# Kernel optimization log

Hardware: AMD Instinct MI355X
Metric: run time of the kernel (lower is better)

## Reference

```python
import jax, jax.numpy as jnp
import numpy as np

EPS = 1e-6
SEARCH_RANGE = 4  # K = 2*R+1 = 9


def setup_inputs() -> dict:
    key = jax.random.key(0)
    k1, k2, k3, k4 = jax.random.split(key, 4)
    B, C, H, W = 4, 128, 128, 240
    E = 64
    F_L = jax.random.normal(k1, (B, C, H, W), dtype=jnp.float32)
    F_R = jax.random.normal(k2, (B, C, H, W), dtype=jnp.float32)
    d0 = jax.random.uniform(k3, (B, 1, H, W), dtype=jnp.float32) * 64.0  # pixel disparity
    phi_w = jax.random.normal(k4, (E, C), dtype=jnp.float32) / np.sqrt(C)  # 1x1 conv weight
    return {"F_L": F_L, "F_R": F_R, "d0": d0, "phi_w": phi_w}


def _embed(x, phi_w):
    # 1x1 conv + channel L2 normalize (cosine embedding)
    y = jnp.einsum('ec,bchw->behw', phi_w, x)
    norm = jnp.sqrt(jnp.sum(y * y, axis=1, keepdims=True)) + EPS
    return y / norm


def reference(F_L, F_R, d0, phi_w):
    R = SEARCH_RANGE
    FL = _embed(F_L, phi_w)  # (B,E,H,W)
    FR = _embed(F_R, phi_w)
    B, E, H, W = FL.shape
    deltas = jnp.arange(-R, R + 1, dtype=FL.dtype)  # (K,)
    xx = jnp.arange(W, dtype=FL.dtype)  # base x grid
    # x' = x - (d0 + delta); align_corners=True grid round-trips to pixel coords exactly,
    # y coordinate is identity, so warp is 1D bilinear along W with border clamp.
    xprime = xx[None, None, None, :] - d0[:, None, 0, :, :] - deltas[None, :, None, None]  # (B,K,H,W)
    x0 = jnp.floor(xprime)
    w = xprime - x0  # bilinear weight
    i0 = jnp.clip(x0.astype(jnp.int32), 0, W - 1)
    i1 = jnp.clip(x0.astype(jnp.int32) + 1, 0, W - 1)
    FR_e = FR[:, None]  # (B,1,E,H,W)
    g0 = jnp.take_along_axis(FR_e, i0[:, :, None, :, :], axis=4)  # (B,K,E,H,W)
    g1 = jnp.take_along_axis(FR_e, i1[:, :, None, :, :], axis=4)
    FR_s = g0 * (1.0 - w)[:, :, None] + g1 * w[:, :, None]
    cost_vol = jnp.einsum('behw,bkehw->bkhw', FL, FR_s)  # (B,K,H,W)
    return cost_vol
```

## Files before the change

### kernel.cpp

```cpp
#include <hip/hip_runtime.h>

#define NB 4
#define NC 128
#define NH 128
#define NW 240
#define NE 64
#define NK 9
#define PLANE (NH*NW)
#define CHW (NC*PLANE)

typedef __attribute__((ext_vector_type(8))) short short8;
typedef __attribute__((ext_vector_type(4))) float f32x4;

__device__ __forceinline__ unsigned short f2bf(float f){
  unsigned u = __float_as_uint(f);
  u += 0x7fffu + ((u>>16)&1u);
  return (unsigned short)(u>>16);
}
__device__ __forceinline__ float bfl(unsigned v){ return __uint_as_float(v<<16); }
__device__ __forceinline__ float bfh(unsigned v){ return __uint_as_float(v & 0xffff0000u); }

__global__ __launch_bounds__(256, 1)
void corr_kernel(const float* __restrict__ xL,
                 const float* __restrict__ xR,
                 const float* __restrict__ d0g,
                 const float* __restrict__ phig,
                 float* __restrict__ outg)
{
  __shared__ __attribute__((aligned(16))) unsigned short stag[NW*136];
  __shared__ __attribute__((aligned(16))) unsigned short phis[NE*136];
  __shared__ __attribute__((aligned(16))) unsigned short FLb[NW*64];
  __shared__ __attribute__((aligned(16))) unsigned short FRb[NW*64];

  const int tid  = threadIdx.x;
  const int lane = tid & 63;
  const int wv   = tid >> 6;
  const int b    = blockIdx.x >> 7;
  const int h    = blockIdx.x & 127;
  const size_t base = (size_t)b*CHW + (size_t)h*NW;

  float4 le0[8], le1[8], lo0[8], lo1[8];
  #pragma unroll
  for (int i = 0; i < 8; ++i) {
    int tau = tid + 256*i;
    if (tau < 1920) {
      int c2 = tau & 63, wo = tau >> 6;
      size_t off = base + (size_t)(2*c2)*PLANE + 8*wo;
      le0[i] = *(const float4*)(xL + off);
      le1[i] = *(const float4*)(xL + off + 4);
      lo0[i] = *(const float4*)(xL + off + PLANE);
      lo1[i] = *(const float4*)(xL + off + PLANE + 4);
    }
  }
  float4 ph[8];
  #pragma unroll
  for (int i = 0; i < 8; ++i) {
    int tau = tid + 256*i;
    int row = tau >> 5, ch = tau & 31;
    ph[i] = *(const float4*)(phig + row*128 + 4*ch);
  }

  #pragma unroll
  for (int i = 0; i < 8; ++i) {
    int tau = tid + 256*i;
    int row = tau >> 5, ch = tau & 31;
    unsigned w0 = (unsigned)f2bf(ph[i].x) | ((unsigned)f2bf(ph[i].y) << 16);
    unsigned w1 = (unsigned)f2bf(ph[i].z) | ((unsigned)f2bf(ph[i].w) << 16);
    uint2 pk; pk.x = w0; pk.y = w1;
    *(uint2*)&phis[row*136 + 4*ch] = pk;
  }
  #pragma unroll
  for (int i = 0; i < 8; ++i) {
    int tau = tid + 256*i;
    if (tau < 1920) {
      int c2 = tau & 63, wo = tau >> 6;
      float fe[8] = {le0[i].x, le0[i].y, le0[i].z, le0[i].w,
                     le1[i].x, le1[i].y, le1[i].z, le1[i].w};
      float fo[8] = {lo0[i].x, lo0[i].y, lo0[i].z, lo0[i].w,
                     lo1[i].x, lo1[i].y, lo1[i].z, lo1[i].w};
      #pragma unroll
      for (int j = 0; j < 8; ++j) {
        unsigned v = (unsigned)f2bf(fe[j]) | ((unsigned)f2bf(fo[j]) << 16);
        *(unsigned*)&stag[(8*wo + j)*136 + 2*c2] = v;
      }
    }
  }
  __syncthreads();

  float4 re0[8], re1[8], ro0[8], ro1[8];
  #pragma unroll
  for (int i = 0; i < 8; ++i) {
    int tau = tid + 256*i;
    if (tau < 1920) {
      int c2 = tau & 63, wo = tau >> 6;
      size_t off = base + (size_t)(2*c2)*PLANE + 8*wo;
      re0[i] = *(const float4*)(xR + off);
      re1[i] = *(const float4*)(xR + off + 4);
      ro0[i] = *(const float4*)(xR + off + PLANE);
      ro1[i] = *(const float4*)(xR + off + PLANE + 4);
    }
  }

  const int mrow = lane & 15;
  const int kg   = lane >> 4;
  const int nt0  = wv*4;

  auto gemm_norm = [&](unsigned short* dst) {
    f32x4 acc[4][4];
    #pragma unroll
    for (int i = 0; i < 4; ++i)
      #pragma unroll
      for (int mt = 0; mt < 4; ++mt)
        acc[i][mt] = (f32x4){0.f,0.f,0.f,0.f};

    #pragma unroll
    for (int ks = 0; ks < 4; ++ks) {
      short8 af[4];
      #pragma unroll
      for (int mt = 0; mt < 4; ++mt)
        af[mt] = *(const short8*)&phis[(16*mt + mrow)*136 + 32*ks + 8*kg];
      #pragma unroll
      for (int i = 0; i < 4; ++i) {
        int nt = nt0 + i;
        if (nt < 15) {
          short8 bfv = *(const short8*)&stag[(16*nt + mrow)*136 + 32*ks + 8*kg];
          #pragma unroll
          for (int mt = 0; mt < 4; ++mt)
            acc[i][mt] = __builtin_amdgcn_mfma_f32_16x16x32_bf16(af[mt], bfv, acc[i][mt], 0, 0, 0);
        }
      }
    }
    #pragma unroll
    for (int i = 0; i < 4; ++i) {
      int nt = nt0 + i;
      if (nt >= 15) continue;
      float ss = 0.f;
      #pragma unroll
      for (int mt = 0; mt < 4; ++mt)
        #pragma unroll
        for (int r = 0; r < 4; ++r)
          ss += acc[i][mt][r]*acc[i][mt][r];
      ss += __shfl_xor(ss, 16, 64);
      ss += __shfl_xor(ss, 32, 64);
      float inv = 1.f/(sqrtf(ss) + 1e-6f);
      int n = 16*nt + mrow;
      #pragma unroll
      for (int mt = 0; mt < 4; ++mt) {
        int e0 = 16*mt + 4*kg;
        ushort4 pk;
        pk.x = f2bf(acc[i][mt][0]*inv);
        pk.y = f2bf(acc[i][mt][1]*inv);
        pk.z = f2bf(acc[i][mt][2]*inv);
        pk.w = f2bf(acc[i][mt][3]*inv);
        int pos = n*64 + (((e0>>3) ^ (n&7))<<3) + (e0&7);
        *(ushort4*)&dst[pos] = pk;
      }
    }
  };

  gemm_norm(FLb);
  __syncthreads();

  #pragma unroll
  for (int i = 0; i < 8; ++i) {
    int tau = tid + 256*i;
    if (tau < 1920) {
      int c2 = tau & 63, wo = tau >> 6;
      float fe[8] = {re0[i].x, re0[i].y, re0[i].z, re0[i].w,
                     re1[i].x, re1[i].y, re1[i].z, re1[i].w};
      float fo[8] = {ro0[i].x, ro0[i].y, ro0[i].z, ro0[i].w,
                     ro1[i].x, ro1[i].y, ro1[i].z, ro1[i].w};
      #pragma unroll
      for (int j = 0; j < 8; ++j) {
        unsigned v = (unsigned)f2bf(fe[j]) | ((unsigned)f2bf(fo[j]) << 16);
        *(unsigned*)&stag[(8*wo + j)*136 + 2*c2] = v;
      }
    }
  }
  __syncthreads();

  gemm_norm(FRb);
  __syncthreads();

  if (tid < NW) {
    const int p = tid;
    float d0v = d0g[(b*NH + h)*NW + p];
    float xf  = (float)p - d0v;
    float x0  = floorf(xf);
    float wfr = xf - x0;
    int jb = (int)x0 - 4;

    float fl[64];
    #pragma unroll
    for (int c = 0; c < 8; ++c) {
      uint4 raw = *(const uint4*)&FLb[p*64 + ((c ^ (p&7))<<3)];
      fl[8*c+0]=bfl(raw.x); fl[8*c+1]=bfh(raw.x);
      fl[8*c+2]=bfl(raw.y); fl[8*c+3]=bfh(raw.y);
      fl[8*c+4]=bfl(raw.z); fl[8*c+5]=bfh(raw.z);
      fl[8*c+6]=bfl(raw.w); fl[8*c+7]=bfh(raw.w);
    }

    float D[10];
    #pragma unroll
    for (int t = 0; t < 10; ++t) {
      int j = jb + t;
      j = j < 0 ? 0 : (j > NW-1 ? NW-1 : j);
      float s = 0.f;
      #pragma unroll
      for (int c = 0; c < 8; ++c) {
        uint4 raw = *(const uint4*)&FRb[j*64 + ((c ^ (j&7))<<3)];
        s += fl[8*c+0]*bfl(raw.x) + fl[8*c+1]*bfh(raw.x)
           + fl[8*c+2]*bfl(raw.y) + fl[8*c+3]*bfh(raw.y)
           + fl[8*c+4]*bfl(raw.z) + fl[8*c+5]*bfh(raw.z)
           + fl[8*c+6]*bfl(raw.w) + fl[8*c+7]*bfh(raw.w);
      }
      D[t] = s;
    }

    size_t ob = (size_t)(b*NK)*PLANE + (size_t)h*NW + p;
    #pragma unroll
    for (int k = 0; k < NK; ++k) {
      int t0 = 8 - k;
      float cv = (1.f - wfr)*D[t0] + wfr*D[t0+1];
      outg[ob + (size_t)k*PLANE] = cv;
    }
  }
}

extern "C" void kernel_launch(void* const* d_in, const int* in_sizes, int n_in,
                              void* d_out, int out_size, void* d_ws, size_t ws_size,
                              hipStream_t stream) {
  const float* xL   = (const float*)d_in[0];
  const float* xR   = (const float*)d_in[1];
  const float* d0g  = (const float*)d_in[2];
  const float* phig = (const float*)d_in[3];
  float* outg = (float*)d_out;
  corr_kernel<<<dim3(NB*NH), dim3(256), 0, stream>>>(xL, xR, d0g, phig, outg);
}
```

Baseline: 174.4 us.

## Stage inputs channel-major in LDS and gather MFMA B fragments per element

```diff
diff --git a/kernel.cpp b/kernel.cpp
--- a/kernel.cpp
+++ b/kernel.cpp
@@ -8,6 +8,7 @@
 #define NK 9
 #define PLANE (NH*NW)
 #define CHW (NC*PLANE)
+#define XS 244
 
 typedef __attribute__((ext_vector_type(8))) short short8;
 typedef __attribute__((ext_vector_type(4))) float f32x4;
@@ -27,7 +28,7 @@
                  const float* __restrict__ phig,
                  float* __restrict__ outg)
 {
-  __shared__ __attribute__((aligned(16))) unsigned short stag[NW*136];
+  __shared__ __attribute__((aligned(16))) unsigned short xs[NC*XS];
   __shared__ __attribute__((aligned(16))) unsigned short phis[NE*136];
   __shared__ __attribute__((aligned(16))) unsigned short FLb[NW*64];
   __shared__ __attribute__((aligned(16))) unsigned short FRb[NW*64];
@@ -39,67 +40,31 @@
   const int h    = blockIdx.x & 127;
   const size_t base = (size_t)b*CHW + (size_t)h*NW;
 
-  float4 le0[8], le1[8], lo0[8], lo1[8];
+  float d0v = 0.f;
+  if (tid < NW) d0v = d0g[(b*NH + h)*NW + tid];
+
   #pragma unroll
   for (int i = 0; i < 8; ++i) {
-    int tau = tid + 256*i;
-    if (tau < 1920) {
-      int c2 = tau & 63, wo = tau >> 6;
-      size_t off = base + (size_t)(2*c2)*PLANE + 8*wo;
-      le0[i] = *(const float4*)(xL + off);
-      le1[i] = *(const float4*)(xL + off + 4);
-      lo0[i] = *(const float4*)(xL + off + PLANE);
-      lo1[i] = *(const float4*)(xL + off + PLANE + 4);
-    }
-  }
-  float4 ph[8];
+    int idx = i*256 + tid;
+    int e = idx >> 5, q = idx & 31;
+    float4 v = *(const float4*)(phig + e*128 + 4*q);
+    uint2 pk;
+    pk.x = (unsigned)f2bf(v.x) | ((unsigned)f2bf(v.y) << 16);
+    pk.y = (unsigned)f2bf(v.z) | ((unsigned)f2bf(v.w) << 16);
+    *(uint2*)&phis[e*136 + 4*q] = pk;
+  }
+
   #pragma unroll
-  for (int i = 0; i < 8; ++i) {
-    int tau = tid + 256*i;
-    int row = tau >> 5, ch = tau & 31;
-    ph[i] = *(const float4*)(phig + row*128 + 4*ch);
-  }
-
-  #pragma unroll
-  for (int i = 0; i < 8; ++i) {
-    int tau = tid + 256*i;
-    int row = tau >> 5, ch = tau & 31;
-    unsigned w0 = (unsigned)f2bf(ph[i].x) | ((unsigned)f2bf(ph[i].y) << 16);
-    unsigned w1 = (unsigned)f2bf(ph[i].z) | ((unsigned)f2bf(ph[i].w) << 16);
-    uint2 pk; pk.x = w0; pk.y = w1;
-    *(uint2*)&phis[row*136 + 4*ch] = pk;
-  }
-  #pragma unroll
-  for (int i = 0; i < 8; ++i) {
-    int tau = tid + 256*i;
-    if (tau < 1920) {
-      int c2 = tau & 63, wo = tau >> 6;
-      float fe[8] = {le0[i].x, le0[i].y, le0[i].z, le0[i].w,
-                     le1[i].x, le1[i].y, le1[i].z, le1[i].w};
-      float fo[8] = {lo0[i].x, lo0[i].y, lo0[i].z, lo0[i].w,
-                     lo1[i].x, lo1[i].y, lo1[i].z, lo1[i].w};
-      #pragma unroll
-      for (int j = 0; j < 8; ++j) {
-        unsigned v = (unsigned)f2bf(fe[j]) | ((unsigned)f2bf(fo[j]) << 16);
-        *(unsigned*)&stag[(8*wo + j)*136 + 2*c2] = v;
-      }
-    }
-  }
-  __syncthreads();
-
-  float4 re0[8], re1[8], ro0[8], ro1[8];
-  #pragma unroll
-  for (int i = 0; i < 8; ++i) {
-    int tau = tid + 256*i;
-    if (tau < 1920) {
-      int c2 = tau & 63, wo = tau >> 6;
-      size_t off = base + (size_t)(2*c2)*PLANE + 8*wo;
-      re0[i] = *(const float4*)(xR + off);
-      re1[i] = *(const float4*)(xR + off + 4);
-      ro0[i] = *(const float4*)(xR + off + PLANE);
-      ro1[i] = *(const float4*)(xR + off + PLANE + 4);
-    }
-  }
+  for (int i = 0; i < 30; ++i) {
+    int idx = i*256 + tid;
+    int c = idx / 60, s = idx - 60*c;
+    float4 v = *(const float4*)(xL + base + (size_t)c*PLANE + 4*s);
+    uint2 pk;
+    pk.x = (unsigned)f2bf(v.x) | ((unsigned)f2bf(v.y) << 16);
+    pk.y = (unsigned)f2bf(v.z) | ((unsigned)f2bf(v.w) << 16);
+    *(uint2*)&xs[c*XS + 4*s] = pk;
+  }
+  __syncthreads();
 
   const int mrow = lane & 15;
   const int kg   = lane >> 4;
@@ -119,11 +84,16 @@
       #pragma unroll
       for (int mt = 0; mt < 4; ++mt)
         af[mt] = *(const short8*)&phis[(16*mt + mrow)*136 + 32*ks + 8*kg];
+      const int r0 = 32*ks + 8*kg;
       #pragma unroll
       for (int i = 0; i < 4; ++i) {
         int nt = nt0 + i;
         if (nt < 15) {
-          short8 bfv = *(const short8*)&stag[(16*nt + mrow)*136 + 32*ks + 8*kg];
+          int col = 16*nt + mrow;
+          short8 bfv;
+          #pragma unroll
+          for (int j = 0; j < 8; ++j)
+            bfv[j] = (short)xs[(r0 + j)*XS + col];
           #pragma unroll
           for (int mt = 0; mt < 4; ++mt)
             acc[i][mt] = __builtin_amdgcn_mfma_f32_16x16x32_bf16(af[mt], bfv, acc[i][mt], 0, 0, 0);
@@ -162,20 +132,14 @@
   __syncthreads();
 
   #pragma unroll
-  for (int i = 0; i < 8; ++i) {
-    int tau = tid + 256*i;
-    if (tau < 1920) {
-      int c2 = tau & 63, wo = tau >> 6;
-      float fe[8] = {re0[i].x, re0[i].y, re0[i].z, re0[i].w,
-                     re1[i].x, re1[i].y, re1[i].z, re1[i].w};
-      float fo[8] = {ro0[i].x, ro0[i].y, ro0[i].z, ro0[i].w,
-                     ro1[i].x, ro1[i].y, ro1[i].z, ro1[i].w};
-      #pragma unroll
-      for (int j = 0; j < 8; ++j) {
-        unsigned v = (unsigned)f2bf(fe[j]) | ((unsigned)f2bf(fo[j]) << 16);
-        *(unsigned*)&stag[(8*wo + j)*136 + 2*c2] = v;
-      }
-    }
+  for (int i = 0; i < 30; ++i) {
+    int idx = i*256 + tid;
+    int c = idx / 60, s = idx - 60*c;
+    float4 v = *(const float4*)(xR + base + (size_t)c*PLANE + 4*s);
+    uint2 pk;
+    pk.x = (unsigned)f2bf(v.x) | ((unsigned)f2bf(v.y) << 16);
+    pk.y = (unsigned)f2bf(v.z) | ((unsigned)f2bf(v.w) << 16);
+    *(uint2*)&xs[c*XS + 4*s] = pk;
   }
   __syncthreads();
 
@@ -184,7 +148,6 @@
 
   if (tid < NW) {
     const int p = tid;
-    float d0v = d0g[(b*NH + h)*NW + p];
     float xf  = (float)p - d0v;
     float x0  = floorf(xf);
     float wfr = xf - x0;
```

New measurement: 160.4 us. 1.09x faster.
